# Kernel tuning notes

Hardware: AMD Instinct MI355X
Metric: run time of the kernel (lower is better)

Reference implementation:

```python
import jax, jax.numpy as jnp
import numpy as np

N_DATASETS = 2
DATASET_CATS = (1536, 1536)
TOTAL_CATS = 3072
MAX_UNIFY = 1536
N_NODES = TOTAL_CATS + MAX_UNIFY  # 4608
LRELU_ALPHA = 0.2
BI_TEMP = 0.05
NEG_INF = -9e15


def setup_inputs() -> dict:
    key = jax.random.key(0)
    ks = jax.random.split(key, 12)
    nfeat, nfeat_out, nfeat_adj, nhid, nheads = 512, 256, 64, 64, 4
    att_out, mlp = 256, 512
    s = lambda k, sh: (jax.random.normal(k, sh, jnp.float32) * 0.05)
    return {
        'x': jax.random.normal(ks[0], (N_NODES, nfeat), jnp.float32),
        'W_before': s(ks[1], (nfeat, nfeat_out)),
        'b_before': jnp.zeros((nfeat_out,), jnp.float32),
        'W_adj': s(ks[2], (nfeat_out, nfeat_adj)),
        'b_adj': jnp.zeros((nfeat_adj,), jnp.float32),
        'W_heads': s(ks[3], (nheads, nfeat_out, nhid)),
        'a_heads': s(ks[4], (nheads, 2 * nhid)),
        'W_out': s(ks[5], (nheads * nhid, att_out)),
        'a_out': s(ks[6], (2 * att_out,)),
        'W_lin1': s(ks[7], (att_out, mlp)),
        'b_lin1': jnp.zeros((mlp,), jnp.float32),
    }


def _calc_adjacency(x_out, W_adj, b_adj):
    # linear_adj + L2 normalize + cosine similarity + row normalization via diag(1/rowsum)
    af = x_out @ W_adj + b_adj                              # [N, nfeat_adj]
    nrm = jnp.sqrt(jnp.sum(af * af, axis=1, keepdims=True))
    naf = af / jnp.maximum(nrm, 1e-12)
    sim = naf @ naf.T                                       # [N, N]
    rowsum = jnp.sum(sim, axis=1)
    r_inv = 1.0 / rowsum
    r_inv = jnp.where(jnp.isinf(r_inv), 0.0, r_inv)
    return r_inv[:, None] * sim                             # diag(1/rowsum) @ sim


def _gat_multihead(x, adj, W, a):
    # W: [H, F, d], a: [H, 2d]. Standard pyGAT dense attention, vectorized over heads.
    d = W.shape[-1]
    Wh = jnp.einsum('nf,hfd->hnd', x, W)                    # [H, N, d]
    f1 = jnp.einsum('hnd,hd->hn', Wh, a[:, :d])             # [H, N]
    f2 = jnp.einsum('hnd,hd->hn', Wh, a[:, d:])             # [H, N]
    e = jax.nn.leaky_relu(f1[:, :, None] + f2[:, None, :], LRELU_ALPHA)  # [H, N, N]
    att = jnp.where(adj[None] > 0, e, NEG_INF)
    att = jax.nn.softmax(att, axis=-1)
    return jnp.einsum('hnm,hmd->hnd', att, Wh)              # [H, N, d]


def _gat_single(x, adj, W, a):
    d = W.shape[-1]
    Wh = x @ W                                              # [N, d]
    f1 = Wh @ a[:d]
    f2 = Wh @ a[d:]
    e = jax.nn.leaky_relu(f1[:, None] + f2[None, :], LRELU_ALPHA)
    att = jnp.where(adj > 0, e, NEG_INF)
    att = jax.nn.softmax(att, axis=-1)
    return att @ Wh


def reference(x, W_before, b_before, W_adj, b_adj, W_heads, a_heads, W_out, a_out, W_lin1, b_lin1):
    x1 = x @ W_before + b_before                            # linear_before
    adj = _calc_adjacency(x1, W_adj, b_adj)                 # before relu, as in source
    x1 = jax.nn.relu(x1)
    # multi-head GAT layer 1 (concat=True -> elu per head, concat along feature dim)
    h = jax.nn.elu(_gat_multihead(x1, adj, W_heads, a_heads))   # [H, N, d]
    H, N, d = h.shape
    feat = jnp.transpose(h, (1, 0, 2)).reshape(N, H * d)
    x2 = feat + x1                                          # residual; dropout is eval no-op
    # output attention head (concat=False -> no elu inside)
    x3 = jax.nn.elu(_gat_single(x2, adj, W_out, a_out) + x2)
    feat_mlp = x3 @ W_lin1 + b_lin1                          # linear1
    # sep_bipartite_graphs: per-dataset column-softmax over unify columns
    bgs = []
    cur = 0
    for nc in DATASET_CATS:
        blk = adj[cur:cur + nc, TOTAL_CATS:]                 # [nc, MAX_UNIFY]
        bgs.append(jax.nn.softmax(blk / BI_TEMP, axis=0))
        cur += nc
    return (feat_mlp[TOTAL_CATS:],) + tuple(bgs)


if __name__ == '__main__':
    out = reference(**setup_inputs())
    for o in out:
        print(o.shape, o.dtype)
```

## Files before the change

kernel.cpp:

```cpp
#include <hip/hip_runtime.h>
#include <hip/hip_bf16.h>
#include <math.h>

constexpr int NTOT = 4608;
constexpr int TC   = 3072;
constexpr int MU   = 1536;
constexpr int NH   = 4;

constexpr long OFF_ADJ  = 0;
constexpr long OFF_X1   = OFF_ADJ  + (long)NTOT*NTOT;
constexpr long OFF_NAF  = OFF_X1   + (long)NTOT*256;
constexpr long OFF_PART = OFF_NAF  + (long)NTOT*64;
constexpr long OFF_RINV = OFF_PART + 72*64;
constexpr long OFF_WH   = OFF_RINV + NTOT;
constexpr long OFF_F1H  = OFF_WH   + (long)4*NTOT*64;
constexpr long OFF_F2H  = OFF_F1H  + (long)4*NTOT;
constexpr long OFF_MXH  = OFF_F2H  + (long)4*NTOT;
constexpr long OFF_CIH  = OFF_MXH  + (long)4*NTOT;
constexpr long OFF_X2   = OFF_CIH  + (long)4*NTOT;
constexpr long OFF_WH2  = OFF_X2   + (long)NTOT*256;
constexpr long OFF_F1S  = OFF_WH2  + (long)NTOT*256;
constexpr long OFF_F2S  = OFF_F1S  + NTOT;
constexpr long OFF_MXS  = OFF_F2S  + NTOT;
constexpr long OFF_CIS  = OFF_MXS  + NTOT;
constexpr long OFF_X3   = OFF_CIS  + NTOT;
constexpr long OFF_PMAX = OFF_X3   + (long)MU*256;
constexpr long OFF_PSUM = OFF_PMAX + (long)2*12*MU;
constexpr long OFF_FMAX = OFF_PSUM + (long)2*12*MU;
constexpr long OFF_FIS  = OFF_FMAX + (long)2*MU;
constexpr long OFF_L1   = OFF_FIS  + (long)2*MU;
constexpr long OFF_L2   = OFF_L1   + (long)4*NTOT;
constexpr long OFF_PARTS = OFF_ADJ + (long)TC*NTOT;
constexpr long OFF_POSB  = OFF_PARTS + 2L*NTOT*36;
constexpr long OFF_MASKB = OFF_POSB  + 2L*NTOT*72;

typedef __attribute__((ext_vector_type(8))) short bf16x8;
typedef __attribute__((ext_vector_type(8))) unsigned short ushort8;
typedef __attribute__((ext_vector_type(4))) float floatx4;

__device__ __forceinline__ float elu(float x)   { return (x > 0.f) ? x : expm1f(x); }
__device__ __forceinline__ unsigned short f2bf(float f) {
    unsigned u = __float_as_uint(f);
    u += 0x7FFFu + ((u >> 16) & 1u);
    return (unsigned short)(u >> 16);
}

__global__ __launch_bounds__(256) void zero2_k(
    float* __restrict__ a, long na4, float* __restrict__ b, long nb4)
{
    long i = (long)blockIdx.x * 256 + threadIdx.x;
    float4 z = make_float4(0.f, 0.f, 0.f, 0.f);
    if (i < na4) *(float4*)(a + i * 4) = z;
    else {
        long j = i - na4;
        if (j < nb4) *(float4*)(b + j * 4) = z;
    }
}

template<bool RELU_A, bool BIAS>
__global__ __launch_bounds__(256) void gemm_rm(
    const float* __restrict__ A, const float* __restrict__ B,
    const float* __restrict__ bias, float* __restrict__ C,
    int K, int M, long strideBz, long strideCz)
{
    __shared__ float As[16][68];
    __shared__ float Bs[16][68];
    const float* Bz = B + (long)blockIdx.z * strideBz;
    float* Cz = C + (long)blockIdx.z * strideCz;
    int tid = threadIdx.x;
    int r0 = blockIdx.x * 64;
    int c0 = blockIdx.y * 64;
    int ty = tid >> 4, tx = tid & 15;
    int srow = tid >> 2, skg = tid & 3;
    int bkk = tid >> 4, bc4 = (tid & 15) * 4;
    const float* Arow = A + (long)(r0 + srow) * K + skg * 4;
    float4 aReg = *(const float4*)(Arow);
    float4 bReg = *(const float4*)&Bz[(long)bkk * M + c0 + bc4];
    float acc[4][4] = {};
    for (int k0 = 0; k0 < K; k0 += 16) {
        {
            float4 v = aReg;
            if (RELU_A) {
                v.x = fmaxf(v.x, 0.f); v.y = fmaxf(v.y, 0.f);
                v.z = fmaxf(v.z, 0.f); v.w = fmaxf(v.w, 0.f);
            }
            As[skg * 4 + 0][srow] = v.x;
            As[skg * 4 + 1][srow] = v.y;
            As[skg * 4 + 2][srow] = v.z;
            As[skg * 4 + 3][srow] = v.w;
            *(float4*)&Bs[bkk][bc4] = bReg;
        }
        __syncthreads();
        if (k0 + 16 < K) {
            aReg = *(const float4*)(Arow + k0 + 16);
            bReg = *(const float4*)&Bz[(long)(k0 + 16 + bkk) * M + c0 + bc4];
        }
        #pragma unroll
        for (int kk = 0; kk < 16; ++kk) {
            float4 av = *(const float4*)&As[kk][ty * 4];
            float4 bv = *(const float4*)&Bs[kk][tx * 4];
            float a[4] = { av.x, av.y, av.z, av.w };
            float b[4] = { bv.x, bv.y, bv.z, bv.w };
            #pragma unroll
            for (int i = 0; i < 4; ++i)
                #pragma unroll
                for (int j = 0; j < 4; ++j) acc[i][j] += a[i] * b[j];
        }
        __syncthreads();
    }
    #pragma unroll
    for (int i = 0; i < 4; ++i) {
        int r = r0 + ty * 4 + i;
        #pragma unroll
        for (int j = 0; j < 4; ++j) {
            int c = c0 + tx * 4 + j;
            float v = acc[i][j];
            if (BIAS) v += bias[c];
            Cz[(long)r * M + c] = v;
        }
    }
}

__global__ __launch_bounds__(256) void af_naf(
    const float* __restrict__ x1, const float* __restrict__ W_adj,
    const float* __restrict__ b_adj, float* __restrict__ nafT)
{
    __shared__ float rowbuf[4][256];
    int tid = threadIdx.x, w = tid >> 6, lane = tid & 63;
    int n = blockIdx.x * 4 + w;
    #pragma unroll
    for (int l = 0; l < 4; ++l) rowbuf[w][l * 64 + lane] = x1[(long)n * 256 + l * 64 + lane];
    __syncthreads();
    float acc = b_adj[lane];
    for (int k = 0; k < 256; ++k) acc += rowbuf[w][k] * W_adj[k * 64 + lane];
    float sq = acc * acc;
    #pragma unroll
    for (int off = 32; off >= 1; off >>= 1) sq += __shfl_xor(sq, off);
    float nrm = fmaxf(sqrtf(sq), 1e-12f);
    nafT[(long)lane * NTOT + n] = acc / nrm;
}

__global__ __launch_bounds__(256) void sim_k8(
    const float* __restrict__ nafT, float* __restrict__ sim,
    double* __restrict__ parts, unsigned long long* __restrict__ posb)
{
    __shared__ float As[32][128];
    __shared__ float Bs[32][128];
    __shared__ unsigned char sgn[128][2][16];
    int tid = threadIdx.x;
    int n0 = blockIdx.x * 128, m0 = blockIdx.y * 128;
    int ty = tid >> 4, tx = tid & 15;
    float acc[2][2][4][4] = {};
    for (int ks = 0; ks < 2; ++ks) {
        if (ks) __syncthreads();
        int k0 = ks * 32;
        #pragma unroll
        for (int l = 0; l < 4; ++l) {
            int idx = l * 256 + tid;
            int kk = idx >> 5, f4 = idx & 31;
            *(float4*)&As[kk][f4 * 4] = *(const float4*)&nafT[(long)(k0 + kk) * NTOT + n0 + f4 * 4];
            *(float4*)&Bs[kk][f4 * 4] = *(const float4*)&nafT[(long)(k0 + kk) * NTOT + m0 + f4 * 4];
        }
        __syncthreads();
        for (int kk = 0; kk < 32; ++kk) {
            float4 av0 = *(const float4*)&As[kk][ty * 4];
            float4 av1 = *(const float4*)&As[kk][64 + ty * 4];
            float4 bv0 = *(const float4*)&Bs[kk][tx * 4];
            float4 bv1 = *(const float4*)&Bs[kk][64 + tx * 4];
            float a[2][4] = { { av0.x, av0.y, av0.z, av0.w }, { av1.x, av1.y, av1.z, av1.w } };
            float b[2][4] = { { bv0.x, bv0.y, bv0.z, bv0.w }, { bv1.x, bv1.y, bv1.z, bv1.w } };
            #pragma unroll
            for (int rh = 0; rh < 2; ++rh)
                #pragma unroll
                for (int ch = 0; ch < 2; ++ch)
                    #pragma unroll
                    for (int i = 0; i < 4; ++i)
                        #pragma unroll
                        for (int j = 0; j < 4; ++j)
                            acc[rh][ch][i][j] += a[rh][i] * b[ch][j];
        }
    }
    if (m0 >= TC && n0 < TC) {
        #pragma unroll
        for (int rh = 0; rh < 2; ++rh)
            #pragma unroll
            for (int i = 0; i < 4; ++i) {
                long r = n0 + rh * 64 + ty * 4 + i;
                #pragma unroll
                for (int ch = 0; ch < 2; ++ch) {
                    float4 o = make_float4(acc[rh][ch][i][0], acc[rh][ch][i][1],
                                           acc[rh][ch][i][2], acc[rh][ch][i][3]);
                    *(float4*)(sim + r * NTOT + m0 + ch * 64 + tx * 4) = o;
                }
            }
    }
    int mt36 = m0 >> 7;
    #pragma unroll
    for (int rh = 0; rh < 2; ++rh)
        #pragma unroll
        for (int i = 0; i < 4; ++i) {
            double t = 0.0;
            #pragma unroll
            for (int ch = 0; ch < 2; ++ch)
                t += ((double)acc[rh][ch][i][0] + (double)acc[rh][ch][i][1])
                   + ((double)acc[rh][ch][i][2] + (double)acc[rh][ch][i][3]);
            #pragma unroll
            for (int off = 1; off < 16; off <<= 1) t += __shfl_xor(t, off);
            if (tx == 0)
                parts[(long)(n0 + rh * 64 + ty * 4 + i) * 36 + mt36] = t;
        }
    int mt = m0 >> 6;
    #pragma unroll
    for (int rh = 0; rh < 2; ++rh)
        #pragma unroll
        for (int i = 0; i < 4; ++i)
            #pragma unroll
            for (int ch = 0; ch < 2; ++ch) {
                unsigned nib = (unsigned)(acc[rh][ch][i][0] > 0.f)
                             | ((unsigned)(acc[rh][ch][i][1] > 0.f) << 1)
                             | ((unsigned)(acc[rh][ch][i][2] > 0.f) << 2)
                             | ((unsigned)(acc[rh][ch][i][3] > 0.f) << 3);
                sgn[rh * 64 + ty * 4 + i][ch][tx] = (unsigned char)nib;
            }
    __syncthreads();
    {
        int rl = tid >> 1, gh = tid & 1;
        unsigned long long w = 0;
        #pragma unroll
        for (int t = 0; t < 16; ++t)
            w |= (unsigned long long)sgn[rl][gh][t] << (4 * t);
        posb[(long)(n0 + rl) * 72 + mt + gh] = w;
    }
}

__global__ __launch_bounds__(256) void fused1(
    const float* __restrict__ Wh, unsigned short* __restrict__ Whbf,
    const float* __restrict__ a_heads,
    float* __restrict__ f1, float* __restrict__ f2,
    float* __restrict__ e2p, float* __restrict__ e2n,
    const double* __restrict__ parts, const unsigned long long* __restrict__ posb,
    float* __restrict__ rinv, unsigned long long* __restrict__ maskb)
{
    __shared__ float t[64][65];
    int b = blockIdx.x;
    int tid = threadIdx.x;
    if (b < 288) {
        int bx = b % 72, bz = b / 72;
        int n0 = bx * 64;
        const float* inz = Wh + (long)bz * NTOT * 64;
        unsigned short* outz = Whbf + (long)bz * 64 * NTOT;
        int r4 = tid >> 6, k = tid & 63;
        #pragma unroll
        for (int l = 0; l < 16; ++l) {
            int row = l * 4 + r4;
            t[row][k] = inz[(long)(n0 + row) * 64 + k];
        }
        __syncthreads();
        #pragma unroll
        for (int l = 0; l < 16; ++l) {
            int drow = l * 4 + r4;
            outz[(long)drow * NTOT + n0 + k] = f2bf(t[k][drow]);
        }
    } else if (b < 288 + 4608) {
        int tb = b - 288;
        int xb = tb % 1152, h = tb / 1152;
        int w = tid >> 6, lane = tid & 63;
        int n = xb * 4 + w;
        const float* row = Wh + ((long)h * NTOT + n) * 64;
        const float* a1 = a_heads + (long)h * 128;
        const float* a2 = a1 + 64;
        float v = row[lane];
        float p1 = v * a1[lane];
        float p2 = v * a2[lane];
        #pragma unroll
        for (int off = 32; off >= 1; off >>= 1) { p1 += __shfl_xor(p1, off); p2 += __shfl_xor(p2, off); }
        if (lane == 0) {
            f1[(long)h * NTOT + n] = p1;
            f2[(long)h * NTOT + n] = p2;
            e2p[(long)h * NTOT + n] = __expf(p2);
            e2n[(long)h * NTOT + n] = __expf(0.2f * p2);
        }
    } else {
        int xb = b - (288 + 4608);
        int w = tid >> 6, lane = tid & 63;
        int n = xb * 4 + w;
        double s = (lane < 36) ? parts[(long)n * 36 + lane] : 0.0;
        #pragma unroll
        for (int off = 32; off >= 1; off >>= 1) s += __shfl_xor(s, off);
        float rs = (float)s;
        float r = 1.0f / rs;
        if (isinf(r)) r = 0.f;
        if (lane == 0) rinv[n] = r;
        unsigned long long pw = posb[(long)n * 72 + lane];
        unsigned long long mw = (r < 0.f) ? ~pw : pw;
        if (r == 0.f) mw = 0ull;
        maskb[(long)n * 72 + lane] = mw;
        if (lane < 8) {
            pw = posb[(long)n * 72 + 64 + lane];
            mw = (r < 0.f) ? ~pw : pw;
            if (r == 0.f) mw = 0ull;
            maskb[(long)n * 72 + 64 + lane] = mw;
        }
    }
}

__global__ __launch_bounds__(256) void fused2(
    const float* __restrict__ Wh2, unsigned short* __restrict__ Wh2bf,
    const float* __restrict__ a_out,
    float* __restrict__ f1, float* __restrict__ f2,
    float* __restrict__ e2p, float* __restrict__ e2n)
{
    __shared__ float t[64][65];
    int b = blockIdx.x;
    int tid = threadIdx.x;
    if (b < 288) {
        int bx = b % 72, by = b / 72;
        int n0 = bx * 64, d0 = by * 64;
        int r4 = tid >> 6, k = tid & 63;
        #pragma unroll
        for (int l = 0; l < 16; ++l) {
            int row = l * 4 + r4;
            t[row][k] = Wh2[(long)(n0 + row) * 256 + d0 + k];
        }
        __syncthreads();
        #pragma unroll
        for (int l = 0; l < 16; ++l) {
            int drow = l * 4 + r4;
            Wh2bf[(long)(d0 + drow) * NTOT + n0 + k] = f2bf(t[k][drow]);
        }
    } else {
        int xb = b - 288;
        int w = tid >> 6, lane = tid & 63;
        int n = xb * 4 + w;
        const float* row = Wh2 + (long)n * 256;
        const float* a1 = a_out;
        const float* a2 = a_out + 256;
        float p1 = 0.f, p2 = 0.f;
        #pragma unroll
        for (int l = 0; l < 4; ++l) {
            float v = row[l * 64 + lane];
            p1 += v * a1[l * 64 + lane];
            p2 += v * a2[l * 64 + lane];
        }
        #pragma unroll
        for (int off = 32; off >= 1; off >>= 1) { p1 += __shfl_xor(p1, off); p2 += __shfl_xor(p2, off); }
        if (lane == 0) {
            f1[n] = p1;
            f2[n] = p2;
            e2p[n] = __expf(p2);
            e2n[n] = __expf(0.2f * p2);
        }
    }
}

__global__ __launch_bounds__(256) void mh_attn(
    const unsigned long long* __restrict__ maskb,
    const float* __restrict__ f1,
    const float* __restrict__ e2p, const float* __restrict__ e2n,
    const unsigned short* __restrict__ Whbf, float* __restrict__ accb,
    float* __restrict__ lbuf)
{
    __shared__ unsigned short Ws[2][64][74];
    int tid = threadIdx.x;
    int wave = tid >> 6, lane = tid & 63;
    int n0 = blockIdx.x * 64;
    int h = blockIdx.y, ch = blockIdx.z;
    const float* Ep = e2p + (long)h * NTOT;
    const float* En = e2n + (long)h * NTOT;
    const unsigned short* Wb = Whbf + (long)h * 64 * NTOT;
    int wd = tid >> 2, wc = (tid & 3) * 16;
    int arow = lane & 15, acol8 = (lane >> 4) * 8;
    int n = n0 + 16 * wave + arow;
    float r1 = f1[(long)h * NTOT + n];
    float e1p = __expf(r1), e1n = __expf(0.2f * r1);
    float lsum = 0.f;
    floatx4 acc[4] = {};
    int buf = 0;
    int mt0 = ch * 12;
    ushort8 wv0 = *(const ushort8*)&Wb[(long)wd * NTOT + mt0 * 64 + wc];
    ushort8 wv1 = *(const ushort8*)&Wb[(long)wd * NTOT + mt0 * 64 + wc + 8];
    unsigned long long mw = maskb[(long)n * 72 + mt0];
    float4 pv0[2], pv1[2], nv0[2], nv1[2];
    #pragma unroll
    for (int ks = 0; ks < 2; ++ks) {
        int mc = mt0 * 64 + ks * 32 + acol8;
        pv0[ks] = *(const float4*)(Ep + mc);
        pv1[ks] = *(const float4*)(Ep + mc + 4);
        nv0[ks] = *(const float4*)(En + mc);
        nv1[ks] = *(const float4*)(En + mc + 4);
    }
    for (int i = 0; i < 12; ++i) {
        bf16x8 afr[2];
        #pragma unroll
        for (int ks = 0; ks < 2; ++ks) {
            unsigned bits = (unsigned)(mw >> (ks * 32 + acol8)) & 0xFFu;
            float fp[8] = { pv0[ks].x, pv0[ks].y, pv0[ks].z, pv0[ks].w,
                            pv1[ks].x, pv1[ks].y, pv1[ks].z, pv1[ks].w };
            float fn[8] = { nv0[ks].x, nv0[ks].y, nv0[ks].z, nv0[ks].w,
                            nv1[ks].x, nv1[ks].y, nv1[ks].z, nv1[ks].w };
            #pragma unroll
            for (int j = 0; j < 8; ++j) {
                float tp = e1p * fp[j];
                float tn = e1n * fn[j];
                float p = (tp >= 1.0f) ? tp : tn;
                p = ((bits >> j) & 1u) ? p : 0.f;
                lsum += p;
                afr[ks][j] = (short)f2bf(p);
            }
        }
        *(ushort8*)&Ws[buf][wd][wc] = wv0;
        *(ushort8*)&Ws[buf][wd][wc + 8] = wv1;
        if (i < 11) {
            int m1 = (mt0 + i + 1) * 64;
            wv0 = *(const ushort8*)&Wb[(long)wd * NTOT + m1 + wc];
            wv1 = *(const ushort8*)&Wb[(long)wd * NTOT + m1 + wc + 8];
            mw = maskb[(long)n * 72 + mt0 + i + 1];
            #pragma unroll
            for (int ks = 0; ks < 2; ++ks) {
                int mc = m1 + ks * 32 + acol8;
                pv0[ks] = *(const float4*)(Ep + mc);
                pv1[ks] = *(const float4*)(Ep + mc + 4);
                nv0[ks] = *(const float4*)(En + mc);
                nv1[ks] = *(const float4*)(En + mc + 4);
            }
        }
        __syncthreads();
        #pragma unroll
        for (int ks = 0; ks < 2; ++ks) {
            #pragma unroll
            for (int dt = 0; dt < 4; ++dt) {
                bf16x8 bfr = *(bf16x8*)&Ws[buf][16 * dt + arow][ks * 32 + acol8];
                acc[dt] = __builtin_amdgcn_mfma_f32_16x16x32_bf16(afr[ks], bfr, acc[dt], 0, 0, 0);
            }
        }
        buf ^= 1;
    }
    lsum += __shfl_xor(lsum, 16);
    lsum += __shfl_xor(lsum, 32);
    if (lane < 16) atomicAdd(lbuf + (long)h * NTOT + n0 + 16 * wave + lane, lsum);
    int crow = n0 + 16 * wave + (lane >> 4) * 4;
    int ccol = h * 64 + (lane & 15);
    #pragma unroll
    for (int dt = 0; dt < 4; ++dt)
        #pragma unroll
        for (int r = 0; r < 4; ++r)
            atomicAdd(accb + (long)(crow + r) * 256 + ccol + dt * 16, acc[dt][r]);
}

__global__ __launch_bounds__(256) void mh_fin(
    const float* __restrict__ accb, const float* __restrict__ lbuf,
    float* __restrict__ x1, float* __restrict__ x2)
{
    long idx = ((long)blockIdx.x * 256 + threadIdx.x) * 4;
    long r = idx >> 8;
    int h = (int)((idx & 255) >> 6);
    float l = lbuf[(long)h * NTOT + r];
    float inv = (l > 0.f) ? 1.0f / l : 0.f;
    float4 a = *(const float4*)(accb + idx);
    float4 xv = *(const float4*)(x1 + idx);
    float4 o;
    o.x = elu(a.x * inv) + fmaxf(xv.x, 0.f);
    o.y = elu(a.y * inv) + fmaxf(xv.y, 0.f);
    o.z = elu(a.z * inv) + fmaxf(xv.z, 0.f);
    o.w = elu(a.w * inv) + fmaxf(xv.w, 0.f);
    *(float4*)(x2 + idx) = o;
    if (idx < (long)MU * 256)
        *(float4*)(x1 + idx) = make_float4(0.f, 0.f, 0.f, 0.f);
}

__global__ __launch_bounds__(256) void s_attn(
    const unsigned long long* __restrict__ maskb,
    const float* __restrict__ f1,
    const float* __restrict__ e2p, const float* __restrict__ e2n,
    const unsigned short* __restrict__ Wh2bf, float* __restrict__ accb,
    float* __restrict__ lbuf)
{
    __shared__ unsigned short Ws[2][128][74];
    int tid = threadIdx.x;
    int wave = tid >> 6, lane = tid & 63;
    int lr0 = blockIdx.x * 32;
    int c0 = blockIdx.y * 128;
    int ch = blockIdx.z;
    int wdl = tid >> 2, wc = (tid & 3) * 16;
    int arow = lane & 15, acol8 = (lane >> 4) * 8;
    int rt = wave & 1;
    int dt0 = (wave >> 1) * 4;
    int n = TC + lr0 + 16 * rt + arow;
    float r1 = f1[n];
    float e1p = __expf(r1), e1n = __expf(0.2f * r1);
    float lsum = 0.f;
    floatx4 acc[4] = {};
    int buf = 0;
    int mt0 = ch * 6;
    ushort8 wva0 = *(const ushort8*)&Wh2bf[(long)(c0 + wdl) * NTOT + mt0 * 64 + wc];
    ushort8 wva1 = *(const ushort8*)&Wh2bf[(long)(c0 + wdl) * NTOT + mt0 * 64 + wc + 8];
    ushort8 wvb0 = *(const ushort8*)&Wh2bf[(long)(c0 + 64 + wdl) * NTOT + mt0 * 64 + wc];
    ushort8 wvb1 = *(const ushort8*)&Wh2bf[(long)(c0 + 64 + wdl) * NTOT + mt0 * 64 + wc + 8];
    unsigned long long mw = maskb[(long)n * 72 + mt0];
    for (int i = 0; i < 6; ++i) {
        int m0 = (mt0 + i) * 64;
        bf16x8 afr[2];
        #pragma unroll
        for (int ks = 0; ks < 2; ++ks) {
            int mc = m0 + ks * 32 + acol8;
            float4 pv0 = *(const float4*)(e2p + mc);
            float4 pv1 = *(const float4*)(e2p + mc + 4);
            float4 nv0 = *(const float4*)(e2n + mc);
            float4 nv1 = *(const float4*)(e2n + mc + 4);
            unsigned bits = (unsigned)(mw >> (ks * 32 + acol8)) & 0xFFu;
            float fp[8] = { pv0.x, pv0.y, pv0.z, pv0.w, pv1.x, pv1.y, pv1.z, pv1.w };
            float fn[8] = { nv0.x, nv0.y, nv0.z, nv0.w, nv1.x, nv1.y, nv1.z, nv1.w };
            #pragma unroll
            for (int j = 0; j < 8; ++j) {
                float tp = e1p * fp[j];
                float tn = e1n * fn[j];
                float p = (tp >= 1.0f) ? tp : tn;
                p = ((bits >> j) & 1u) ? p : 0.f;
                lsum += p;
                afr[ks][j] = (short)f2bf(p);
            }
        }
        *(ushort8*)&Ws[buf][wdl][wc] = wva0;
        *(ushort8*)&Ws[buf][wdl][wc + 8] = wva1;
        *(ushort8*)&Ws[buf][64 + wdl][wc] = wvb0;
        *(ushort8*)&Ws[buf][64 + wdl][wc + 8] = wvb1;
        if (i < 5) {
            int m1 = (mt0 + i + 1) * 64;
            wva0 = *(const ushort8*)&Wh2bf[(long)(c0 + wdl) * NTOT + m1 + wc];
            wva1 = *(const ushort8*)&Wh2bf[(long)(c0 + wdl) * NTOT + m1 + wc + 8];
            wvb0 = *(const ushort8*)&Wh2bf[(long)(c0 + 64 + wdl) * NTOT + m1 + wc];
            wvb1 = *(const ushort8*)&Wh2bf[(long)(c0 + 64 + wdl) * NTOT + m1 + wc + 8];
            mw = maskb[(long)n * 72 + mt0 + i + 1];
        }
        __syncthreads();
        #pragma unroll
        for (int ks = 0; ks < 2; ++ks) {
            #pragma unroll
            for (int t = 0; t < 4; ++t) {
                bf16x8 bfr = *(bf16x8*)&Ws[buf][(dt0 + t) * 16 + arow][ks * 32 + acol8];
                acc[t] = __builtin_amdgcn_mfma_f32_16x16x32_bf16(afr[ks], bfr, acc[t], 0, 0, 0);
            }
        }
        buf ^= 1;
    }
    lsum += __shfl_xor(lsum, 16);
    lsum += __shfl_xor(lsum, 32);
    if (blockIdx.y == 0 && wave < 2 && lane < 16)
        atomicAdd(lbuf + lr0 + 16 * wave + lane, lsum);
    int crow = lr0 + 16 * rt + (lane >> 4) * 4;
    #pragma unroll
    for (int t = 0; t < 4; ++t) {
        int ccol = c0 + (dt0 + t) * 16 + (lane & 15);
        #pragma unroll
        for (int r = 0; r < 4; ++r)
            atomicAdd(accb + (long)(crow + r) * 256 + ccol, acc[t][r]);
    }
}

__global__ __launch_bounds__(256) void s_fin(
    const float* __restrict__ accb, const float* __restrict__ lbuf,
    const float* __restrict__ x2, float* __restrict__ x3)
{
    long idx = ((long)blockIdx.x * 256 + threadIdx.x) * 4;
    long r = idx >> 8;
    float l = lbuf[r];
    float inv = (l > 0.f) ? 1.0f / l : 0.f;
    float4 a = *(const float4*)(accb + idx);
    float4 xv = *(const float4*)(x2 + (long)TC * 256 + idx);
    float4 o;
    o.x = elu(a.x * inv + xv.x);
    o.y = elu(a.y * inv + xv.y);
    o.z = elu(a.z * inv + xv.z);
    o.w = elu(a.w * inv + xv.w);
    *(float4*)(x3 + idx) = o;
}

__global__ __launch_bounds__(256) void bi_partial(
    const float* __restrict__ sim, const float* __restrict__ rinv,
    float* __restrict__ pmax, float* __restrict__ psum)
{
    int c = blockIdx.x * 256 + threadIdx.x;
    int ch = blockIdx.y;
    int ds = blockIdx.z;
    float m = -3.0e38f, s = 0.f;
    int rbase = ds * MU + ch * 128;
    for (int r = 0; r < 128; ++r) {
        float a = sim[(long)(rbase + r) * NTOT + TC + c] * rinv[rbase + r];
        float v = a * 20.0f;
        if (v <= m) s += expf(v - m);
        else { s = s * expf(m - v) + 1.f; m = v; }
    }
    pmax[((long)ds * 12 + ch) * MU + c] = m;
    psum[((long)ds * 12 + ch) * MU + c] = s;
}

__global__ __launch_bounds__(256) void bi_combine(
    const float* __restrict__ pmax, const float* __restrict__ psum,
    float* __restrict__ fmax, float* __restrict__ fis)
{
    int b = blockIdx.x;
    int ds = b / 6, ct = b % 6;
    int c = ct * 256 + threadIdx.x;
    float m = -3.0e38f;
    for (int ch = 0; ch < 12; ++ch) m = fmaxf(m, pmax[((long)ds * 12 + ch) * MU + c]);
    float s = 0.f;
    for (int ch = 0; ch < 12; ++ch)
        s += psum[((long)ds * 12 + ch) * MU + c] * expf(pmax[((long)ds * 12 + ch) * MU + c] - m);
    fmax[ds * MU + c] = m;
    fis[ds * MU + c] = 1.0f / s;
}

__global__ __launch_bounds__(256) void bi_norm(
    const float* __restrict__ sim, const float* __restrict__ rinv,
    const float* __restrict__ fmax, const float* __restrict__ fis,
    float* __restrict__ outbg)
{
    int c = blockIdx.x * 256 + threadIdx.x;
    int ch = blockIdx.y;
    int ds = blockIdx.z;
    float m = fmax[ds * MU + c], inv = fis[ds * MU + c];
    long obase = (long)ds * MU * MU;
    int rbase = ch * 128;
    for (int r = 0; r < 128; ++r) {
        int row = ds * MU + rbase + r;
        float a = sim[(long)row * NTOT + TC + c] * rinv[row];
        float v = a * 20.0f;
        outbg[obase + (long)(rbase + r) * MU + c] = expf(v - m) * inv;
    }
}

extern "C" void kernel_launch(void* const* d_in, const int* in_sizes, int n_in,
                              void* d_out, int out_size, void* d_ws, size_t ws_size,
                              hipStream_t stream)
{
    const float* x        = (const float*)d_in[0];
    const float* W_before = (const float*)d_in[1];
    const float* b_before = (const float*)d_in[2];
    const float* W_adj    = (const float*)d_in[3];
    const float* b_adj    = (const float*)d_in[4];
    const float* W_heads  = (const float*)d_in[5];
    const float* a_heads  = (const float*)d_in[6];
    const float* W_out    = (const float*)d_in[7];
    const float* a_out    = (const float*)d_in[8];
    const float* W_lin1   = (const float*)d_in[9];
    const float* b_lin1   = (const float*)d_in[10];
    float* out = (float*)d_out;
    float* ws  = (float*)d_ws;

    float* sim  = ws + OFF_ADJ;
    float* x1p  = ws + OFF_X1;
    float* nafT = ws + OFF_NAF;
    float* rinv = ws + OFF_RINV;
    float* Wh   = ws + OFF_WH;
    float* f1h  = ws + OFF_F1H;
    float* f2h  = ws + OFF_F2H;
    float* e2ph = ws + OFF_MXH;
    float* e2nh = ws + OFF_CIH;
    float* x2   = ws + OFF_X2;
    float* Wh2  = ws + OFF_WH2;
    float* f1s  = ws + OFF_F1S;
    float* f2s  = ws + OFF_F2S;
    float* e2sp = ws + OFF_MXS;
    float* e2sn = ws + OFF_CIS;
    float* x3   = ws + OFF_X3;
    float* pmax = ws + OFF_PMAX;
    float* psum = ws + OFF_PSUM;
    float* fmx  = ws + OFF_FMAX;
    float* fis  = ws + OFF_FIS;
    float* l1   = ws + OFF_L1;
    float* l2   = ws + OFF_L2;
    float* acc1 = ws + OFF_WH2;
    float* acc2 = ws + OFF_X1;
    unsigned short* Whbf  = (unsigned short*)(ws + OFF_X2);
    unsigned short* Wh2bf = (unsigned short*)(ws + OFF_X1 + (long)MU * 256);
    double* parts = (double*)(ws + OFF_PARTS);
    unsigned long long* posb  = (unsigned long long*)(ws + OFF_POSB);
    unsigned long long* maskb = (unsigned long long*)(ws + OFF_MASKB);

    dim3 b256(256);

    zero2_k<<<dim3(1172), b256, 0, stream>>>(acc1, (long)NTOT * 64, l1, 5120);
    gemm_rm<false, true><<<dim3(72, 4, 1), b256, 0, stream>>>(x, W_before, b_before, x1p, 512, 256, 0, 0);
    af_naf<<<dim3(1152), b256, 0, stream>>>(x1p, W_adj, b_adj, nafT);
    sim_k8<<<dim3(36, 36), b256, 0, stream>>>(nafT, sim, parts, posb);
    gemm_rm<true, false><<<dim3(72, 1, 4), b256, 0, stream>>>(x1p, W_heads, nullptr, Wh, 256, 64,
                                                              (long)256 * 64, (long)NTOT * 64);
    fused1<<<dim3(288 + 4608 + 1152), b256, 0, stream>>>(Wh, Whbf, a_heads, f1h, f2h, e2ph, e2nh,
                                                         parts, posb, rinv, maskb);
    mh_attn<<<dim3(72, 4, 6), b256, 0, stream>>>(maskb, f1h, e2ph, e2nh, Whbf, acc1, l1);
    mh_fin<<<dim3(NTOT * 256 / 1024), b256, 0, stream>>>(acc1, l1, x1p, x2);
    gemm_rm<false, false><<<dim3(72, 4, 1), b256, 0, stream>>>(x2, W_out, nullptr, Wh2, 256, 256, 0, 0);
    fused2<<<dim3(288 + 1152), b256, 0, stream>>>(Wh2, Wh2bf, a_out, f1s, f2s, e2sp, e2sn);
    s_attn<<<dim3(48, 2, 12), b256, 0, stream>>>(maskb, f1s, e2sp, e2sn, Wh2bf, acc2, l2);
    s_fin<<<dim3(MU * 256 / 1024), b256, 0, stream>>>(acc2, l2, x2, x3);
    gemm_rm<false, true><<<dim3(24, 8, 1), b256, 0, stream>>>(x3, W_lin1, b_lin1, out, 256, 512, 0, 0);
    bi_partial<<<dim3(6, 12, 2), b256, 0, stream>>>(sim, rinv, pmax, psum);
    bi_combine<<<dim3(12), b256, 0, stream>>>(pmax, psum, fmx, fis);
    bi_norm<<<dim3(6, 12, 2), b256, 0, stream>>>(sim, rinv, fmx, fis, out + (long)MU * 512);
}
```

Baseline: 376.2 us.

## Compute attention exponentials inline and transpose bitmask layout for coalesced loads

Instead of precomputing exp(f2) and exp(0.2*f2) per column and multiplying by per-row factors, the attention kernels now load raw f2 and compute exp(leaky_relu(f1+f2)) directly. This halves the per-tile column vector loads and drops the prefetch registers for them. The mask is stored transposed (tile-major by node), so lanes reading consecutive nodes get coalesced 64-bit loads. LDS padding is also trimmed from 74 to 72. The trade-off is one extra exp per element in the inner loop, and the reduced padding may add LDS bank conflicts.

```diff
diff --git a/kernel.cpp b/kernel.cpp
--- a/kernel.cpp
+++ b/kernel.cpp
@@ -237,9 +237,8 @@
     const float* __restrict__ Wh, unsigned short* __restrict__ Whbf,
     const float* __restrict__ a_heads,
     float* __restrict__ f1, float* __restrict__ f2,
-    float* __restrict__ e2p, float* __restrict__ e2n,
     const double* __restrict__ parts, const unsigned long long* __restrict__ posb,
-    float* __restrict__ rinv, unsigned long long* __restrict__ maskb)
+    float* __restrict__ rinv, unsigned long long* __restrict__ maskT)
 {
     __shared__ float t[64][65];
     int b = blockIdx.x;
@@ -277,8 +276,6 @@
         if (lane == 0) {
             f1[(long)h * NTOT + n] = p1;
             f2[(long)h * NTOT + n] = p2;
-            e2p[(long)h * NTOT + n] = __expf(p2);
-            e2n[(long)h * NTOT + n] = __expf(0.2f * p2);
         }
     } else {
         int xb = b - (288 + 4608);
@@ -294,12 +291,12 @@
         unsigned long long pw = posb[(long)n * 72 + lane];
         unsigned long long mw = (r < 0.f) ? ~pw : pw;
         if (r == 0.f) mw = 0ull;
-        maskb[(long)n * 72 + lane] = mw;
+        maskT[(long)lane * NTOT + n] = mw;
         if (lane < 8) {
             pw = posb[(long)n * 72 + 64 + lane];
             mw = (r < 0.f) ? ~pw : pw;
             if (r == 0.f) mw = 0ull;
-            maskb[(long)n * 72 + 64 + lane] = mw;
+            maskT[(long)(64 + lane) * NTOT + n] = mw;
         }
     }
 }
@@ -307,8 +304,7 @@
 __global__ __launch_bounds__(256) void fused2(
     const float* __restrict__ Wh2, unsigned short* __restrict__ Wh2bf,
     const float* __restrict__ a_out,
-    float* __restrict__ f1, float* __restrict__ f2,
-    float* __restrict__ e2p, float* __restrict__ e2n)
+    float* __restrict__ f1, float* __restrict__ f2)
 {
     __shared__ float t[64][65];
     int b = blockIdx.x;
@@ -347,63 +343,49 @@
         if (lane == 0) {
             f1[n] = p1;
             f2[n] = p2;
-            e2p[n] = __expf(p2);
-            e2n[n] = __expf(0.2f * p2);
         }
     }
 }
 
 __global__ __launch_bounds__(256) void mh_attn(
-    const unsigned long long* __restrict__ maskb,
-    const float* __restrict__ f1,
-    const float* __restrict__ e2p, const float* __restrict__ e2n,
+    const unsigned long long* __restrict__ maskT,
+    const float* __restrict__ f1, const float* __restrict__ f2,
     const unsigned short* __restrict__ Whbf, float* __restrict__ accb,
     float* __restrict__ lbuf)
 {
-    __shared__ unsigned short Ws[2][64][74];
+    __shared__ unsigned short Ws[2][64][72];
     int tid = threadIdx.x;
     int wave = tid >> 6, lane = tid & 63;
     int n0 = blockIdx.x * 64;
     int h = blockIdx.y, ch = blockIdx.z;
-    const float* Ep = e2p + (long)h * NTOT;
-    const float* En = e2n + (long)h * NTOT;
+    const float* f2h = f2 + (long)h * NTOT;
     const unsigned short* Wb = Whbf + (long)h * 64 * NTOT;
     int wd = tid >> 2, wc = (tid & 3) * 16;
     int arow = lane & 15, acol8 = (lane >> 4) * 8;
     int n = n0 + 16 * wave + arow;
     float r1 = f1[(long)h * NTOT + n];
-    float e1p = __expf(r1), e1n = __expf(0.2f * r1);
     float lsum = 0.f;
     floatx4 acc[4] = {};
     int buf = 0;
     int mt0 = ch * 12;
     ushort8 wv0 = *(const ushort8*)&Wb[(long)wd * NTOT + mt0 * 64 + wc];
     ushort8 wv1 = *(const ushort8*)&Wb[(long)wd * NTOT + mt0 * 64 + wc + 8];
-    unsigned long long mw = maskb[(long)n * 72 + mt0];
-    float4 pv0[2], pv1[2], nv0[2], nv1[2];
-    #pragma unroll
-    for (int ks = 0; ks < 2; ++ks) {
-        int mc = mt0 * 64 + ks * 32 + acol8;
-        pv0[ks] = *(const float4*)(Ep + mc);
-        pv1[ks] = *(const float4*)(Ep + mc + 4);
-        nv0[ks] = *(const float4*)(En + mc);
-        nv1[ks] = *(const float4*)(En + mc + 4);
-    }
+    unsigned long long mw = maskT[(long)mt0 * NTOT + n];
     for (int i = 0; i < 12; ++i) {
+        int m0 = (mt0 + i) * 64;
         bf16x8 afr[2];
         #pragma unroll
         for (int ks = 0; ks < 2; ++ks) {
+            int mc = m0 + ks * 32 + acol8;
+            float4 fv0 = *(const float4*)(f2h + mc);
+            float4 fv1 = *(const float4*)(f2h + mc + 4);
             unsigned bits = (unsigned)(mw >> (ks * 32 + acol8)) & 0xFFu;
-            float fp[8] = { pv0[ks].x, pv0[ks].y, pv0[ks].z, pv0[ks].w,
-                            pv1[ks].x, pv1[ks].y, pv1[ks].z, pv1[ks].w };
-            float fn[8] = { nv0[ks].x, nv0[ks].y, nv0[ks].z, nv0[ks].w,
-                            nv1[ks].x, nv1[ks].y, nv1[ks].z, nv1[ks].w };
+            float f[8] = { fv0.x, fv0.y, fv0.z, fv0.w, fv1.x, fv1.y, fv1.z, fv1.w };
             #pragma unroll
             for (int j = 0; j < 8; ++j) {
-                float tp = e1p * fp[j];
-                float tn = e1n * fn[j];
-                float p = (tp >= 1.0f) ? tp : tn;
-                p = ((bits >> j) & 1u) ? p : 0.f;
+                float s = r1 + f[j];
+                float e = __expf(fmaxf(s, 0.2f * s));
+                float p = ((bits >> j) & 1u) ? e : 0.f;
                 lsum += p;
                 afr[ks][j] = (short)f2bf(p);
             }
@@ -414,15 +396,7 @@
             int m1 = (mt0 + i + 1) * 64;
             wv0 = *(const ushort8*)&Wb[(long)wd * NTOT + m1 + wc];
             wv1 = *(const ushort8*)&Wb[(long)wd * NTOT + m1 + wc + 8];
-            mw = maskb[(long)n * 72 + mt0 + i + 1];
-            #pragma unroll
-            for (int ks = 0; ks < 2; ++ks) {
-                int mc = m1 + ks * 32 + acol8;
-                pv0[ks] = *(const float4*)(Ep + mc);
-                pv1[ks] = *(const float4*)(Ep + mc + 4);
-                nv0[ks] = *(const float4*)(En + mc);
-                nv1[ks] = *(const float4*)(En + mc + 4);
-            }
+            mw = maskT[(long)(mt0 + i + 1) * NTOT + n];
         }
         __syncthreads();
         #pragma unroll
@@ -469,13 +443,12 @@
 }
 
 __global__ __launch_bounds__(256) void s_attn(
-    const unsigned long long* __restrict__ maskb,
-    const float* __restrict__ f1,
-    const float* __restrict__ e2p, const float* __restrict__ e2n,
+    const unsigned long long* __restrict__ maskT,
+    const float* __restrict__ f1, const float* __restrict__ f2,
     const unsigned short* __restrict__ Wh2bf, float* __restrict__ accb,
     float* __restrict__ lbuf)
 {
-    __shared__ unsigned short Ws[2][128][74];
+    __shared__ unsigned short Ws[2][128][72];
     int tid = threadIdx.x;
     int wave = tid >> 6, lane = tid & 63;
     int lr0 = blockIdx.x * 32;
@@ -487,7 +460,6 @@
     int dt0 = (wave >> 1) * 4;
     int n = TC + lr0 + 16 * rt + arow;
     float r1 = f1[n];
-    float e1p = __expf(r1), e1n = __expf(0.2f * r1);
     float lsum = 0.f;
     floatx4 acc[4] = {};
     int buf = 0;
@@ -496,26 +468,22 @@
     ushort8 wva1 = *(const ushort8*)&Wh2bf[(long)(c0 + wdl) * NTOT + mt0 * 64 + wc + 8];
     ushort8 wvb0 = *(const ushort8*)&Wh2bf[(long)(c0 + 64 + wdl) * NTOT + mt0 * 64 + wc];
     ushort8 wvb1 = *(const ushort8*)&Wh2bf[(long)(c0 + 64 + wdl) * NTOT + mt0 * 64 + wc + 8];
-    unsigned long long mw = maskb[(long)n * 72 + mt0];
+    unsigned long long mw = maskT[(long)mt0 * NTOT + n];
     for (int i = 0; i < 6; ++i) {
         int m0 = (mt0 + i) * 64;
         bf16x8 afr[2];
         #pragma unroll
         for (int ks = 0; ks < 2; ++ks) {
             int mc = m0 + ks * 32 + acol8;
-            float4 pv0 = *(const float4*)(e2p + mc);
-            float4 pv1 = *(const float4*)(e2p + mc + 4);
-            float4 nv0 = *(const float4*)(e2n + mc);
-            float4 nv1 = *(const float4*)(e2n + mc + 4);
+            float4 fv0 = *(const float4*)(f2 + mc);
+            float4 fv1 = *(const float4*)(f2 + mc + 4);
             unsigned bits = (unsigned)(mw >> (ks * 32 + acol8)) & 0xFFu;
-            float fp[8] = { pv0.x, pv0.y, pv0.z, pv0.w, pv1.x, pv1.y, pv1.z, pv1.w };
-            float fn[8] = { nv0.x, nv0.y, nv0.z, nv0.w, nv1.x, nv1.y, nv1.z, nv1.w };
+            float f[8] = { fv0.x, fv0.y, fv0.z, fv0.w, fv1.x, fv1.y, fv1.z, fv1.w };
             #pragma unroll
             for (int j = 0; j < 8; ++j) {
-                float tp = e1p * fp[j];
-                float tn = e1n * fn[j];
-                float p = (tp >= 1.0f) ? tp : tn;
-                p = ((bits >> j) & 1u) ? p : 0.f;
+                float s = r1 + f[j];
+                float e = __expf(fmaxf(s, 0.2f * s));
+                float p = ((bits >> j) & 1u) ? e : 0.f;
                 lsum += p;
                 afr[ks][j] = (short)f2bf(p);
             }
@@ -530,7 +498,7 @@
             wva1 = *(const ushort8*)&Wh2bf[(long)(c0 + wdl) * NTOT + m1 + wc + 8];
             wvb0 = *(const ushort8*)&Wh2bf[(long)(c0 + 64 + wdl) * NTOT + m1 + wc];
             wvb1 = *(const ushort8*)&Wh2bf[(long)(c0 + 64 + wdl) * NTOT + m1 + wc + 8];
-            mw = maskb[(long)n * 72 + mt0 + i + 1];
+            mw = maskT[(long)(mt0 + i + 1) * NTOT + n];
         }
         __syncthreads();
         #pragma unroll
@@ -654,14 +622,10 @@
     float* Wh   = ws + OFF_WH;
     float* f1h  = ws + OFF_F1H;
     float* f2h  = ws + OFF_F2H;
-    float* e2ph = ws + OFF_MXH;
-    float* e2nh = ws + OFF_CIH;
     float* x2   = ws + OFF_X2;
     float* Wh2  = ws + OFF_WH2;
     float* f1s  = ws + OFF_F1S;
     float* f2s  = ws + OFF_F2S;
-    float* e2sp = ws + OFF_MXS;
-    float* e2sn = ws + OFF_CIS;
     float* x3   = ws + OFF_X3;
     float* pmax = ws + OFF_PMAX;
     float* psum = ws + OFF_PSUM;
@@ -675,7 +639,7 @@
     unsigned short* Wh2bf = (unsigned short*)(ws + OFF_X1 + (long)MU * 256);
     double* parts = (double*)(ws + OFF_PARTS);
     unsigned long long* posb  = (unsigned long long*)(ws + OFF_POSB);
-    unsigned long long* maskb = (unsigned long long*)(ws + OFF_MASKB);
+    unsigned long long* maskT = (unsigned long long*)(ws + OFF_MASKB);
 
     dim3 b256(256);
 
@@ -685,13 +649,13 @@
     sim_k8<<<dim3(36, 36), b256, 0, stream>>>(nafT, sim, parts, posb);
     gemm_rm<true, false><<<dim3(72, 1, 4), b256, 0, stream>>>(x1p, W_heads, nullptr, Wh, 256, 64,
                                                               (long)256 * 64, (long)NTOT * 64);
-    fused1<<<dim3(288 + 4608 + 1152), b256, 0, stream>>>(Wh, Whbf, a_heads, f1h, f2h, e2ph, e2nh,
-                                                         parts, posb, rinv, maskb);
-    mh_attn<<<dim3(72, 4, 6), b256, 0, stream>>>(maskb, f1h, e2ph, e2nh, Whbf, acc1, l1);
+    fused1<<<dim3(288 + 4608 + 1152), b256, 0, stream>>>(Wh, Whbf, a_heads, f1h, f2h,
+                                                         parts, posb, rinv, maskT);
+    mh_attn<<<dim3(72, 4, 6), b256, 0, stream>>>(maskT, f1h, f2h, Whbf, acc1, l1);
     mh_fin<<<dim3(NTOT * 256 / 1024), b256, 0, stream>>>(acc1, l1, x1p, x2);
     gemm_rm<false, false><<<dim3(72, 4, 1), b256, 0, stream>>>(x2, W_out, nullptr, Wh2, 256, 256, 0, 0);
-    fused2<<<dim3(288 + 1152), b256, 0, stream>>>(Wh2, Wh2bf, a_out, f1s, f2s, e2sp, e2sn);
-    s_attn<<<dim3(48, 2, 12), b256, 0, stream>>>(maskb, f1s, e2sp, e2sn, Wh2bf, acc2, l2);
+    fused2<<<dim3(288 + 1152), b256, 0, stream>>>(Wh2, Wh2bf, a_out, f1s, f2s);
+    s_attn<<<dim3(48, 2, 12), b256, 0, stream>>>(maskT, f1s, f2s, Wh2bf, acc2, l2);
     s_fin<<<dim3(MU * 256 / 1024), b256, 0, stream>>>(acc2, l2, x2, x3);
     gemm_rm<false, true><<<dim3(24, 8, 1), b256, 0, stream>>>(x3, W_lin1, b_lin1, out, 256, 512, 0, 0);
     bi_partial<<<dim3(6, 12, 2), b256, 0, stream>>>(sim, rinv, pmax, psum);
```

Measured after the change: 379.5 us. About the same (+0.9%).
